# Performance work log

Hardware: AMD Instinct MI355X
Metric: run time of the kernel (lower is better)

## Reference

```python
import jax, jax.numpy as jnp
import numpy as np

B, T, V, H, F = 128, 20, 10000, 512, 49


def _uniform(key, shape, fan):
    s = 1.0 / np.sqrt(fan)
    return jax.random.uniform(key, shape, jnp.float32, -s, s)


def setup_inputs() -> dict:
    key = jax.random.key(0)
    ks = jax.random.split(key, 16)
    return {
        "caption_inputs": jax.random.randint(ks[0], (B, T), 0, V),
        "global_features": jax.random.normal(ks[1], (B, H), jnp.float32),
        "area_features": jax.random.normal(ks[2], (B, H, F), jnp.float32),
        "h0": jnp.zeros((B, H), jnp.float32),
        "c0": jnp.zeros((B, H), jnp.float32),
        # learned params
        "embedding": jax.random.normal(ks[3], (V, H), jnp.float32),
        "W_ih": _uniform(ks[4], (2 * H, 4 * H), H),   # LSTMCell input weights (x @ W_ih)
        "W_hh": _uniform(ks[5], (H, 4 * H), H),
        "b_ih": _uniform(ks[6], (4 * H,), H),
        "b_hh": _uniform(ks[7], (4 * H,), H),
        "Wv": _uniform(ks[8], (H, H), H),             # attention comp_visual
        "Wh": _uniform(ks[9], (H, H), H),             # attention comp_hidden
        "wo": _uniform(ks[10], (H,), H),              # attention output_layer
        "W_out": _uniform(ks[11], (2 * H, V), 2 * H), # decoder output layer
        "b_out": _uniform(ks[12], (V,), 2 * H),
    }


def reference(caption_inputs, global_features, area_features, h0, c0,
              embedding, W_ih, W_hh, b_ih, b_hh, Wv, Wh, wo, W_out, b_out):
    # Precompute attention visual projection (time-invariant): [B,F,H]
    feat = jnp.swapaxes(area_features, 1, 2)          # [B,F,H]
    Vproj = jnp.einsum('bfh,hk->bfk', feat, Wv)       # [B,F,H]
    bias = b_ih + b_hh

    def step(carry, tok):
        h, c = carry
        emb = embedding[tok]                           # [B,H]
        x = jnp.concatenate([emb, global_features], axis=1)   # [B,2H]
        gates = x @ W_ih + h @ W_hh + bias             # [B,4H]
        i, f, g, o = jnp.split(gates, 4, axis=1)
        c = jax.nn.sigmoid(f) * c + jax.nn.sigmoid(i) * jnp.tanh(g)
        h = jax.nn.sigmoid(o) * jnp.tanh(c)
        # spatial attention over F locations
        z = jnp.tanh(Vproj + (h @ Wh)[:, None, :])     # [B,F,H]
        scores = jnp.einsum('bfh,h->bf', z, wo)        # [B,F]
        alpha = jax.nn.softmax(scores, axis=1)
        attended = jnp.einsum('bhf,bf->bh', area_features, alpha)  # [B,H]
        out = jnp.concatenate([h, attended], axis=1) @ W_out + b_out  # [B,V]
        return (h, c), out

    (_, _), outs = jax.lax.scan(step, (h0, c0), caption_inputs.T)  # [T,B,V]
    return jnp.swapaxes(outs, 0, 1)                    # [B,T,V]
```

## Files before the change

kernel.cpp:

```cpp
#include <hip/hip_runtime.h>

#define B_ 128
#define T_ 20
#define V_ 10000
#define H_ 512
#define F_ 49
#define NBLK_ 128

typedef unsigned short u16;
typedef __attribute__((ext_vector_type(8))) short short8;
typedef __attribute__((ext_vector_type(4))) float floatx4;

#define GLOBAL_AS __attribute__((address_space(1)))
#define LDS_AS    __attribute__((address_space(3)))

__device__ inline void load_lds16(const void* g, void* l) {
    __builtin_amdgcn_global_load_lds((const GLOBAL_AS void*)g, (LDS_AS void*)l, 16, 0, 0);
}

__device__ inline u16 f2b(float v) {
    unsigned u = __builtin_bit_cast(unsigned, v);
    unsigned rounding = 0x7FFFu + ((u >> 16) & 1u);
    return (u16)((u + rounding) >> 16);
}
__device__ inline float b2f(u16 h) {
    unsigned u = ((unsigned)h) << 16;
    return __builtin_bit_cast(float, u);
}
__device__ inline float fast_tanh(float x) {
    return 1.f - 2.f / (__expf(2.f * x) + 1.f);
}
__device__ inline float sigm(float x) { return 1.f / (1.f + __expf(-x)); }

__device__ __forceinline__ void tr32(const float* __restrict__ src, u16* __restrict__ dst,
                                     int K, int N, int bx, int by, int tx, int ty,
                                     float (*tile)[33]) {
    int n0 = bx * 32, k0 = by * 32;
    #pragma unroll
    for (int i = 0; i < 32; i += 8) {
        int k = k0 + ty + i, n = n0 + tx;
        tile[ty + i][tx] = (k < K && n < N) ? src[(size_t)k * N + n] : 0.f;
    }
    __syncthreads();
    #pragma unroll
    for (int i = 0; i < 32; i += 8) {
        int n = n0 + ty + i, k = k0 + tx;
        if (n < N && k < K) dst[(size_t)n * K + k] = f2b(tile[tx][ty + i]);
    }
}

__global__ __launch_bounds__(256) void preamble(
        const float* __restrict__ W_ih, const float* __restrict__ W_hh,
        const float* __restrict__ Wv, const float* __restrict__ Wh,
        const float* __restrict__ W_out, const int* __restrict__ cap,
        const float* __restrict__ emb, const float* __restrict__ gf,
        const float* __restrict__ area, const float* __restrict__ h0,
        u16* __restrict__ WihT, u16* __restrict__ WhhT, u16* __restrict__ WvT,
        u16* __restrict__ WhT, u16* __restrict__ WoutT, u16* __restrict__ X,
        u16* __restrict__ feat, u16* __restrict__ Hall, int* __restrict__ bar) {
    __shared__ float tile[32][33];
    const int bid = blockIdx.x, tid = threadIdx.x;
    const int tx = tid & 31, ty = tid >> 5;

    if (bid < 2048) {
        int r = bid;                 tr32(W_ih, WihT, 1024, 2048, r % 64, r / 64, tx, ty, tile);
    } else if (bid < 3072) {
        int r = bid - 2048;          tr32(W_hh, WhhT, 512, 2048, r % 64, r / 64, tx, ty, tile);
    } else if (bid < 3328) {
        int r = bid - 3072;          tr32(Wv, WvT, 512, 512, r % 16, r / 16, tx, ty, tile);
    } else if (bid < 3584) {
        int r = bid - 3328;          tr32(Wh, WhT, 512, 512, r % 16, r / 16, tx, ty, tile);
    } else if (bid < 13600) {
        int r = bid - 3584;          tr32(W_out, WoutT, 1024, 10000, r % 313, r / 313, tx, ty, tile);
    } else if (bid < 16160) {
        int r = bid - 13600;
        int t = r / B_, b = r % B_;
        int tok = cap[b * T_ + t];
        for (int col = tid; col < 2 * H_; col += 256) {
            float v = (col < H_) ? emb[(size_t)tok * H_ + col] : gf[(size_t)b * H_ + (col - H_)];
            X[(size_t)r * (2 * H_) + col] = f2b(v);
        }
    } else if (bid < 19296) {
        int r = bid - 16160;
        #pragma unroll
        for (int k = 0; k < 4; ++k) {
            int idx = r * 1024 + k * 256 + tid;
            int h = idx & (H_ - 1);
            int bf_ = idx >> 9;
            int f = bf_ % F_, b = bf_ / F_;
            feat[idx] = f2b(area[((size_t)b * H_ + h) * F_ + f]);
        }
    } else {
        int r = bid - 19296;
        int i = r * 256 + tid;
        Hall[i] = f2b(h0[i]);
        if (r == 0) bar[tid] = 0;
    }
}

__device__ inline void grid_sync_mg(int* base, int ep) {
    __syncthreads();
    if (threadIdx.x == 0) {
        int old = __hip_atomic_fetch_add(&base[0], 1, __ATOMIC_ACQ_REL, __HIP_MEMORY_SCOPE_AGENT);
        if (old == ep * 32 - 1)
            __hip_atomic_store(&base[32], ep, __ATOMIC_RELEASE, __HIP_MEMORY_SCOPE_AGENT);
        while (__hip_atomic_load(&base[32], __ATOMIC_RELAXED, __HIP_MEMORY_SCOPE_AGENT) < ep)
            __builtin_amdgcn_s_sleep(2);
        (void)__hip_atomic_load(&base[32], __ATOMIC_ACQUIRE, __HIP_MEMORY_SCOPE_AGENT);
    }
    __syncthreads();
}

__global__ __launch_bounds__(256, 1) void decode_loop(
        const u16* __restrict__ WhhT, const float* __restrict__ Xin,
        const float* __restrict__ c0, u16* __restrict__ Hall,
        int* __restrict__ bar) {

    __shared__ __align__(16) u16 Whs[64 * 512];
    __shared__ __align__(16) u16 hstage[32 * 512];
    __shared__ float gl[4 * 32 * 16];
    __shared__ float csh[32 * 16];

    const int tid = threadIdx.x;
    const int wave = tid >> 6, lane = tid & 63;
    const int lm = lane & 15, q = lane >> 4;
    const int bid = blockIdx.x;
    const int jg = bid >> 2, mg = bid & 3;
    int* mybar = bar + mg * 64;

    const int lb0 = tid >> 4, jj = tid & 15;
    const int lb1 = lb0 + 16;
    const int grow0 = mg * 32 + lb0, grow1 = mg * 32 + lb1;
    const int j = jg * 16 + jj;

    #pragma unroll
    for (int i = 0; i < 16; ++i) {
        int row = i * 4 + wave;
        int g = row >> 4, lr = row & 15;
        int grr = g * H_ + jg * 16 + lr;
        load_lds16(WhhT + (size_t)grr * H_ + (size_t)(lane ^ (row & 7)) * 8,
                   (char*)Whs + row * 1024);
    }
    csh[tid] = c0[(size_t)grow0 * H_ + j];
    csh[tid + 256] = c0[(size_t)grow1 * H_ + j];

    float xf[8];
    {
        const float* x0 = Xin + (size_t)grow0 * (4 * H_);
        const float* x1 = Xin + (size_t)grow1 * (4 * H_);
        xf[0] = x0[j]; xf[1] = x0[H_ + j]; xf[2] = x0[2 * H_ + j]; xf[3] = x0[3 * H_ + j];
        xf[4] = x1[j]; xf[5] = x1[H_ + j]; xf[6] = x1[2 * H_ + j]; xf[7] = x1[3 * H_ + j];
    }

    for (int t = 0; t < T_; ++t) {
        const u16* hprev = Hall + (size_t)t * B_ * H_;
        u16* hnext = Hall + (size_t)(t + 1) * B_ * H_;

        #pragma unroll
        for (int it = 0; it < 8; ++it) {
            int row = it * 4 + wave;
            load_lds16(hprev + (size_t)(mg * 32 + row) * H_ + (size_t)(lane ^ (row & 7)) * 8,
                       (char*)hstage + row * 1024);
        }
        __syncthreads();

        floatx4 acc0 = {0.f, 0.f, 0.f, 0.f}, acc1 = {0.f, 0.f, 0.f, 0.f};
        #pragma unroll
        for (int kt = 0; kt < 16; ++kt) {
            int ch = kt * 4 + q;
            short8 a0 = *(const short8*)&hstage[(lm << 9) + ((ch ^ (lm & 7)) << 3)];
            short8 a1 = *(const short8*)&hstage[((16 + lm) << 9) + ((ch ^ (lm & 7)) << 3)];
            short8 bb = *(const short8*)&Whs[((wave * 16 + lm) << 9) + ((ch ^ (lm & 7)) << 3)];
            acc0 = __builtin_amdgcn_mfma_f32_16x16x32_bf16(a0, bb, acc0, 0, 0, 0);
            acc1 = __builtin_amdgcn_mfma_f32_16x16x32_bf16(a1, bb, acc1, 0, 0, 0);
        }
        #pragma unroll
        for (int r = 0; r < 4; ++r) {
            gl[wave * 512 + (q * 4 + r) * 16 + lm] = acc0[r];
            gl[wave * 512 + (16 + q * 4 + r) * 16 + lm] = acc1[r];
        }
        __syncthreads();

        float xc[8];
        #pragma unroll
        for (int i = 0; i < 8; ++i) xc[i] = xf[i];
        if (t + 1 < T_) {
            const float* x0 = Xin + ((size_t)(t + 1) * B_ + grow0) * (4 * H_);
            const float* x1 = Xin + ((size_t)(t + 1) * B_ + grow1) * (4 * H_);
            xf[0] = x0[j]; xf[1] = x0[H_ + j]; xf[2] = x0[2 * H_ + j]; xf[3] = x0[3 * H_ + j];
            xf[4] = x1[j]; xf[5] = x1[H_ + j]; xf[6] = x1[2 * H_ + j]; xf[7] = x1[3 * H_ + j];
        }

        {
            float gi = gl[0 * 512 + lb0 * 16 + jj] + xc[0];
            float gf = gl[1 * 512 + lb0 * 16 + jj] + xc[1];
            float gg = gl[2 * 512 + lb0 * 16 + jj] + xc[2];
            float go = gl[3 * 512 + lb0 * 16 + jj] + xc[3];
            float cn = sigm(gf) * csh[tid] + sigm(gi) * fast_tanh(gg);
            csh[tid] = cn;
            hnext[(size_t)grow0 * H_ + j] = f2b(sigm(go) * fast_tanh(cn));
        }
        {
            float gi = gl[0 * 512 + lb1 * 16 + jj] + xc[4];
            float gf = gl[1 * 512 + lb1 * 16 + jj] + xc[5];
            float gg = gl[2 * 512 + lb1 * 16 + jj] + xc[6];
            float go = gl[3 * 512 + lb1 * 16 + jj] + xc[7];
            float cn = sigm(gf) * csh[tid + 256] + sigm(gi) * fast_tanh(gg);
            csh[tid + 256] = cn;
            hnext[(size_t)grow1 * H_ + j] = f2b(sigm(go) * fast_tanh(cn));
        }

        if (t + 1 < T_) grid_sync_mg(mybar, t + 1);
    }
}

__global__ __launch_bounds__(256) void attn_post(
        const float* __restrict__ ahbuf, const u16* __restrict__ Vprojb,
        const u16* __restrict__ feat, const float* __restrict__ wo,
        const u16* __restrict__ Hall, u16* __restrict__ Hcat) {
    __shared__ __align__(16) u16 Vsh[F_ * H_];
    __shared__ __align__(16) u16 fsh[F_ * H_];
    __shared__ float ash[H_];
    __shared__ float wosh[H_];
    __shared__ float sc[64];

    const int tid = threadIdx.x;
    const int wave = tid >> 6, lane = tid & 63;
    const int b = blockIdx.x >> 1, th = blockIdx.x & 1;

    const short8* vsrc = (const short8*)(Vprojb + (size_t)b * F_ * H_);
    const short8* fsrc = (const short8*)(feat + (size_t)b * F_ * H_);
    for (int i = tid; i < F_ * H_ / 8; i += 256) {
        ((short8*)Vsh)[i] = vsrc[i];
        ((short8*)fsh)[i] = fsrc[i];
    }
    for (int i = tid; i < H_; i += 256) wosh[i] = wo[i];
    __syncthreads();

    for (int t = th * (T_ / 2); t < (th + 1) * (T_ / 2); ++t) {
        for (int i = tid; i < H_; i += 256)
            ash[i] = ahbuf[((size_t)t * B_ + b) * H_ + i];
        __syncthreads();

        for (int f = wave; f < F_; f += 4) {
            short8 vv = *(const short8*)&Vsh[f * H_ + lane * 8];
            float s = 0.f;
            #pragma unroll
            for (int e = 0; e < 8; ++e) {
                int h = lane * 8 + e;
                s += wosh[h] * fast_tanh(b2f((u16)vv[e]) + ash[h]);
            }
            #pragma unroll
            for (int off = 32; off; off >>= 1) s += __shfl_xor(s, off);
            if (lane == 0) sc[f] = s;
        }
        __syncthreads();

        if (tid < 64) {
            float v = (tid < F_) ? sc[tid] : -1e30f;
            float m = v;
            #pragma unroll
            for (int off = 32; off; off >>= 1) m = fmaxf(m, __shfl_xor(m, off));
            float e = (tid < F_) ? __expf(v - m) : 0.f;
            float sum = e;
            #pragma unroll
            for (int off = 32; off; off >>= 1) sum += __shfl_xor(sum, off);
            if (tid < F_) sc[tid] = e / sum;
        }
        __syncthreads();

        const size_t rowo = ((size_t)b * T_ + t) * (2 * H_);
        const short8* hrow = (const short8*)(Hall + ((size_t)(t + 1) * B_ + b) * H_);
        for (int i = tid; i < H_ / 8; i += 256)
            ((short8*)(Hcat + rowo))[i] = hrow[i];
        for (int h = tid; h < H_; h += 256) {
            float acc = 0.f;
            #pragma unroll
            for (int f = 0; f < F_; ++f) acc += b2f(fsh[f * H_ + h]) * sc[f];
            Hcat[rowo + H_ + h] = f2b(acc);
        }
        __syncthreads();
    }
}

template <int WRITE_BF16>
__device__ __forceinline__ void gemm2_body(
        const u16* __restrict__ A, int lda, const u16* __restrict__ Bt, int ldb,
        void* __restrict__ Cout, int ldc, const float* __restrict__ bias1,
        const float* __restrict__ bias2, int M, int N, int K, int bx, int by,
        u16* As, u16* Bs) {
    const int tid = threadIdx.x, wave = tid >> 6, lane = tid & 63;
    const int wr = wave >> 1, wc = wave & 1;
    const int lm = lane & 15, q = lane >> 4;
    const int m0 = bx * 128, n0 = by * 128;

    const int off = wave * 1024 + lane * 16;
    const int r0 = off >> 6;
    const int c0 = (off & 63) >> 1;

    const u16* gA0 = A + (size_t)(m0 + r0) * lda + c0;
    const u16* gA1 = A + (size_t)(m0 + r0 + 64) * lda + c0;
    int nb0 = n0 + r0;      if (nb0 > N - 1) nb0 = N - 1;
    int nb1 = n0 + r0 + 64; if (nb1 > N - 1) nb1 = N - 1;
    const u16* gB0 = Bt + (size_t)nb0 * ldb + c0;
    const u16* gB1 = Bt + (size_t)nb1 * ldb + c0;
    char* lA0 = (char*)As + wave * 1024;
    char* lA1 = (char*)As + 4096 + wave * 1024;
    char* lB0 = (char*)Bs + wave * 1024;
    char* lB1 = (char*)Bs + 4096 + wave * 1024;

    floatx4 acc[4][4];
    #pragma unroll
    for (int i = 0; i < 4; ++i)
        #pragma unroll
        for (int jq = 0; jq < 4; ++jq) acc[i][jq] = floatx4{0.f, 0.f, 0.f, 0.f};

    const int nkt = K >> 5;
    for (int kt = 0; kt < nkt; ++kt) {
        const int ko = kt * 32;
        load_lds16(gA0 + ko, lA0);
        load_lds16(gA1 + ko, lA1);
        load_lds16(gB0 + ko, lB0);
        load_lds16(gB1 + ko, lB1);
        __syncthreads();
        short8 af[4], bf[4];
        #pragma unroll
        for (int i = 0; i < 4; ++i)
            af[i] = *(const short8*)&As[(wr * 64 + i * 16 + lm) * 32 + q * 8];
        #pragma unroll
        for (int jq = 0; jq < 4; ++jq)
            bf[jq] = *(const short8*)&Bs[(wc * 64 + jq * 16 + lm) * 32 + q * 8];
        #pragma unroll
        for (int i = 0; i < 4; ++i)
            #pragma unroll
            for (int jq = 0; jq < 4; ++jq)
                acc[i][jq] = __builtin_amdgcn_mfma_f32_16x16x32_bf16(af[i], bf[jq], acc[i][jq], 0, 0, 0);
        __syncthreads();
    }

    #pragma unroll
    for (int i = 0; i < 4; ++i) {
        const int row = m0 + wr * 64 + i * 16 + q * 4;
        #pragma unroll
        for (int jq = 0; jq < 4; ++jq) {
            const int col = n0 + wc * 64 + jq * 16 + lm;
            if (col < N) {
                #pragma unroll
                for (int r = 0; r < 4; ++r) {
                    float v = acc[i][jq][r];
                    if (bias1) v += bias1[col];
                    if (bias2) v += bias2[col];
                    if (WRITE_BF16) ((u16*)Cout)[(size_t)(row + r) * ldc + col] = f2b(v);
                    else            ((float*)Cout)[(size_t)(row + r) * ldc + col] = v;
                }
            }
        }
    }
}

template <int WRITE_BF16>
__global__ __launch_bounds__(256) void gemm2(const u16* __restrict__ A, int lda,
                                             const u16* __restrict__ Bt, int ldb,
                                             void* __restrict__ Cout, int ldc,
                                             const float* __restrict__ bias1,
                                             const float* __restrict__ bias2,
                                             int M, int N, int K) {
    __shared__ __align__(16) u16 As[128 * 32];
    __shared__ __align__(16) u16 Bs[128 * 32];
    gemm2_body<WRITE_BF16>(A, lda, Bt, ldb, Cout, ldc, bias1, bias2, M, N, K,
                           blockIdx.x, blockIdx.y, As, Bs);
}

__global__ __launch_bounds__(256) void gemm_pair(
        const u16* __restrict__ X, const u16* __restrict__ WihT,
        float* __restrict__ Xin, const float* __restrict__ b_ih,
        const float* __restrict__ b_hh, const u16* __restrict__ feat,
        const u16* __restrict__ WvT, u16* __restrict__ Vprojb) {
    __shared__ __align__(16) u16 As[128 * 32];
    __shared__ __align__(16) u16 Bs[128 * 32];
    int bid = blockIdx.x;
    if (bid < 320) {
        gemm2_body<0>(X, 2 * H_, WihT, 2 * H_, Xin, 4 * H_, b_ih, b_hh,
                      T_ * B_, 4 * H_, 2 * H_, bid % 20, bid / 20, As, Bs);
    } else {
        int r = bid - 320;
        gemm2_body<1>(feat, H_, WvT, H_, Vprojb, H_, nullptr, nullptr,
                      B_ * F_, H_, H_, r % 49, r / 49, As, Bs);
    }
}

extern "C" void kernel_launch(void* const* d_in, const int* in_sizes, int n_in,
                              void* d_out, int out_size, void* d_ws, size_t ws_size,
                              hipStream_t stream) {
    const int*   cap   = (const int*)d_in[0];
    const float* gf    = (const float*)d_in[1];
    const float* area  = (const float*)d_in[2];
    const float* h0    = (const float*)d_in[3];
    const float* c0    = (const float*)d_in[4];
    const float* emb   = (const float*)d_in[5];
    const float* W_ih  = (const float*)d_in[6];
    const float* W_hh  = (const float*)d_in[7];
    const float* b_ih  = (const float*)d_in[8];
    const float* b_hh  = (const float*)d_in[9];
    const float* Wv    = (const float*)d_in[10];
    const float* Wh    = (const float*)d_in[11];
    const float* wo    = (const float*)d_in[12];
    const float* W_out = (const float*)d_in[13];
    const float* b_out = (const float*)d_in[14];
    float* out = (float*)d_out;

    char* p = (char*)d_ws;
    auto alloc = [&](size_t bytes) {
        char* q = p;
        p += (bytes + 255) & ~(size_t)255;
        return q;
    };
    u16*   X      = (u16*)alloc((size_t)T_ * B_ * 2 * H_ * 2);
    u16*   WihT   = (u16*)alloc((size_t)4 * H_ * 2 * H_ * 2);
    u16*   WhhT   = (u16*)alloc((size_t)4 * H_ * H_ * 2);
    u16*   WvT    = (u16*)alloc((size_t)H_ * H_ * 2);
    u16*   WhT    = (u16*)alloc((size_t)H_ * H_ * 2);
    u16*   WoutT  = (u16*)alloc((size_t)V_ * 2 * H_ * 2);
    u16*   feat   = (u16*)alloc((size_t)B_ * F_ * H_ * 2);
    float* Xin    = (float*)alloc((size_t)T_ * B_ * 4 * H_ * 4);
    u16*   Vprojb = (u16*)alloc((size_t)B_ * F_ * H_ * 2);
    float* ahbuf  = (float*)alloc((size_t)T_ * B_ * H_ * 4);
    u16*   Hall   = (u16*)alloc((size_t)(T_ + 1) * B_ * H_ * 2);
    int*   bar    = (int*)alloc(1024);
    u16*   Hcat   = (u16*)alloc((size_t)B_ * T_ * 2 * H_ * 2);

    preamble<<<19552, 256, 0, stream>>>(W_ih, W_hh, Wv, Wh, W_out, cap, emb, gf,
                                        area, h0, WihT, WhhT, WvT, WhT, WoutT,
                                        X, feat, Hall, bar);

    gemm_pair<<<516, 256, 0, stream>>>(X, WihT, Xin, b_ih, b_hh, feat, WvT, Vprojb);

    decode_loop<<<NBLK_, 256, 0, stream>>>(WhhT, Xin, c0, Hall, bar);

    gemm2<0><<<dim3(T_ * B_ / 128, H_ / 128), 256, 0, stream>>>(
        Hall + (size_t)B_ * H_, H_, WhT, H_, ahbuf, H_, nullptr, nullptr, T_ * B_, H_, H_);

    attn_post<<<2 * B_, 256, 0, stream>>>(ahbuf, Vprojb, feat, wo, Hall, Hcat);

    gemm2<0><<<dim3(T_ * B_ / 128, (V_ + 127) / 128), 256, 0, stream>>>(
        Hcat, 2 * H_, WoutT, 2 * H_, out, V_, b_out, nullptr, T_ * B_, V_, 2 * H_);
}
```

Baseline: 601.3 us.

## Double-buffer GEMM LDS tiles, remap blocks per XCD, tile the feature transpose

The GEMM body now prefetches the next K-slice into a second LDS buffer while MFMAs consume the current one, which removes one barrier per iteration. gemm2 remaps workgroup ids so that consecutive tiles land on the same XCD, aiming for better L2 reuse. The area-feature bf16 conversion now uses the 32x32 shared-memory transpose instead of strided scalar reads. The cost is doubled LDS use per block, which may reduce occupancy.

Measured after the change: 587.3 us. 2.3% less time.

```diff
diff --git a/kernel.cpp b/kernel.cpp
--- a/kernel.cpp
+++ b/kernel.cpp
@@ -34,18 +34,18 @@
 
 __device__ __forceinline__ void tr32(const float* __restrict__ src, u16* __restrict__ dst,
                                      int K, int N, int bx, int by, int tx, int ty,
-                                     float (*tile)[33]) {
+                                     float (*tl)[33]) {
     int n0 = bx * 32, k0 = by * 32;
     #pragma unroll
     for (int i = 0; i < 32; i += 8) {
         int k = k0 + ty + i, n = n0 + tx;
-        tile[ty + i][tx] = (k < K && n < N) ? src[(size_t)k * N + n] : 0.f;
+        tl[ty + i][tx] = (k < K && n < N) ? src[(size_t)k * N + n] : 0.f;
     }
     __syncthreads();
     #pragma unroll
     for (int i = 0; i < 32; i += 8) {
         int n = n0 + ty + i, k = k0 + tx;
-        if (n < N && k < K) dst[(size_t)n * K + k] = f2b(tile[tx][ty + i]);
+        if (n < N && k < K) dst[(size_t)n * K + k] = f2b(tl[tx][ty + i]);
     }
 }
 
@@ -58,20 +58,20 @@
         u16* __restrict__ WihT, u16* __restrict__ WhhT, u16* __restrict__ WvT,
         u16* __restrict__ WhT, u16* __restrict__ WoutT, u16* __restrict__ X,
         u16* __restrict__ feat, u16* __restrict__ Hall, int* __restrict__ bar) {
-    __shared__ float tile[32][33];
+    __shared__ float tl[32][33];
     const int bid = blockIdx.x, tid = threadIdx.x;
     const int tx = tid & 31, ty = tid >> 5;
 
     if (bid < 2048) {
-        int r = bid;                 tr32(W_ih, WihT, 1024, 2048, r % 64, r / 64, tx, ty, tile);
+        int r = bid;                 tr32(W_ih, WihT, 1024, 2048, r % 64, r / 64, tx, ty, tl);
     } else if (bid < 3072) {
-        int r = bid - 2048;          tr32(W_hh, WhhT, 512, 2048, r % 64, r / 64, tx, ty, tile);
+        int r = bid - 2048;          tr32(W_hh, WhhT, 512, 2048, r % 64, r / 64, tx, ty, tl);
     } else if (bid < 3328) {
-        int r = bid - 3072;          tr32(Wv, WvT, 512, 512, r % 16, r / 16, tx, ty, tile);
+        int r = bid - 3072;          tr32(Wv, WvT, 512, 512, r % 16, r / 16, tx, ty, tl);
     } else if (bid < 3584) {
-        int r = bid - 3328;          tr32(Wh, WhT, 512, 512, r % 16, r / 16, tx, ty, tile);
+        int r = bid - 3328;          tr32(Wh, WhT, 512, 512, r % 16, r / 16, tx, ty, tl);
     } else if (bid < 13600) {
-        int r = bid - 3584;          tr32(W_out, WoutT, 1024, 10000, r % 313, r / 313, tx, ty, tile);
+        int r = bid - 3584;          tr32(W_out, WoutT, 1024, 10000, r % 313, r / 313, tx, ty, tl);
     } else if (bid < 16160) {
         int r = bid - 13600;
         int t = r / B_, b = r % B_;
@@ -80,18 +80,14 @@
             float v = (col < H_) ? emb[(size_t)tok * H_ + col] : gf[(size_t)b * H_ + (col - H_)];
             X[(size_t)r * (2 * H_) + col] = f2b(v);
         }
-    } else if (bid < 19296) {
+    } else if (bid < 20256) {
         int r = bid - 16160;
-        #pragma unroll
-        for (int k = 0; k < 4; ++k) {
-            int idx = r * 1024 + k * 256 + tid;
-            int h = idx & (H_ - 1);
-            int bf_ = idx >> 9;
-            int f = bf_ % F_, b = bf_ / F_;
-            feat[idx] = f2b(area[((size_t)b * H_ + h) * F_ + f]);
-        }
+        int b = r >> 5, t32 = r & 31;
+        int fx = t32 & 1, hy = t32 >> 1;
+        tr32(area + (size_t)b * H_ * F_, feat + (size_t)b * F_ * H_,
+             H_, F_, fx, hy, tx, ty, tl);
     } else {
-        int r = bid - 19296;
+        int r = bid - 20256;
         int i = r * 256 + tid;
         Hall[i] = f2b(h0[i]);
         if (r == 0) bar[tid] = 0;
@@ -304,10 +300,6 @@
     int nb1 = n0 + r0 + 64; if (nb1 > N - 1) nb1 = N - 1;
     const u16* gB0 = Bt + (size_t)nb0 * ldb + c0;
     const u16* gB1 = Bt + (size_t)nb1 * ldb + c0;
-    char* lA0 = (char*)As + wave * 1024;
-    char* lA1 = (char*)As + 4096 + wave * 1024;
-    char* lB0 = (char*)Bs + wave * 1024;
-    char* lB1 = (char*)Bs + 4096 + wave * 1024;
 
     floatx4 acc[4][4];
     #pragma unroll
@@ -316,26 +308,41 @@
         for (int jq = 0; jq < 4; ++jq) acc[i][jq] = floatx4{0.f, 0.f, 0.f, 0.f};
 
     const int nkt = K >> 5;
+    {
+        load_lds16(gA0, (char*)As + wave * 1024);
+        load_lds16(gA1, (char*)As + 4096 + wave * 1024);
+        load_lds16(gB0, (char*)Bs + wave * 1024);
+        load_lds16(gB1, (char*)Bs + 4096 + wave * 1024);
+    }
+    __syncthreads();
+
+    int cur = 0;
     for (int kt = 0; kt < nkt; ++kt) {
-        const int ko = kt * 32;
-        load_lds16(gA0 + ko, lA0);
-        load_lds16(gA1 + ko, lA1);
-        load_lds16(gB0 + ko, lB0);
-        load_lds16(gB1 + ko, lB1);
-        __syncthreads();
+        if (kt + 1 < nkt) {
+            const int ko = (kt + 1) * 32;
+            char* dA = (char*)(As + (cur ^ 1) * 4096);
+            char* dB = (char*)(Bs + (cur ^ 1) * 4096);
+            load_lds16(gA0 + ko, dA + wave * 1024);
+            load_lds16(gA1 + ko, dA + 4096 + wave * 1024);
+            load_lds16(gB0 + ko, dB + wave * 1024);
+            load_lds16(gB1 + ko, dB + 4096 + wave * 1024);
+        }
+        const u16* Ab = As + cur * 4096;
+        const u16* Bb = Bs + cur * 4096;
         short8 af[4], bf[4];
         #pragma unroll
         for (int i = 0; i < 4; ++i)
-            af[i] = *(const short8*)&As[(wr * 64 + i * 16 + lm) * 32 + q * 8];
+            af[i] = *(const short8*)&Ab[(wr * 64 + i * 16 + lm) * 32 + q * 8];
         #pragma unroll
         for (int jq = 0; jq < 4; ++jq)
-            bf[jq] = *(const short8*)&Bs[(wc * 64 + jq * 16 + lm) * 32 + q * 8];
+            bf[jq] = *(const short8*)&Bb[(wc * 64 + jq * 16 + lm) * 32 + q * 8];
         #pragma unroll
         for (int i = 0; i < 4; ++i)
             #pragma unroll
             for (int jq = 0; jq < 4; ++jq)
                 acc[i][jq] = __builtin_amdgcn_mfma_f32_16x16x32_bf16(af[i], bf[jq], acc[i][jq], 0, 0, 0);
         __syncthreads();
+        cur ^= 1;
     }
 
     #pragma unroll
@@ -365,10 +372,16 @@
                                              const float* __restrict__ bias1,
                                              const float* __restrict__ bias2,
                                              int M, int N, int K) {
-    __shared__ __align__(16) u16 As[128 * 32];
-    __shared__ __align__(16) u16 Bs[128 * 32];
+    __shared__ __align__(16) u16 As[2 * 128 * 32];
+    __shared__ __align__(16) u16 Bs[2 * 128 * 32];
+    const int nbx = gridDim.x;
+    const int nwg = nbx * gridDim.y;
+    const int lin = blockIdx.x + blockIdx.y * nbx;
+    const int qq = nwg >> 3, rr = nwg & 7;
+    const int xcd = lin & 7, idx = lin >> 3;
+    const int wg = (xcd < rr ? xcd * (qq + 1) : rr * (qq + 1) + (xcd - rr) * qq) + idx;
     gemm2_body<WRITE_BF16>(A, lda, Bt, ldb, Cout, ldc, bias1, bias2, M, N, K,
-                           blockIdx.x, blockIdx.y, As, Bs);
+                           wg % nbx, wg / nbx, As, Bs);
 }
 
 __global__ __launch_bounds__(256) void gemm_pair(
@@ -376,8 +389,8 @@
         float* __restrict__ Xin, const float* __restrict__ b_ih,
         const float* __restrict__ b_hh, const u16* __restrict__ feat,
         const u16* __restrict__ WvT, u16* __restrict__ Vprojb) {
-    __shared__ __align__(16) u16 As[128 * 32];
-    __shared__ __align__(16) u16 Bs[128 * 32];
+    __shared__ __align__(16) u16 As[2 * 128 * 32];
+    __shared__ __align__(16) u16 Bs[2 * 128 * 32];
     int bid = blockIdx.x;
     if (bid < 320) {
         gemm2_body<0>(X, 2 * H_, WihT, 2 * H_, Xin, 4 * H_, b_ih, b_hh,
@@ -429,7 +442,7 @@
     int*   bar    = (int*)alloc(1024);
     u16*   Hcat   = (u16*)alloc((size_t)B_ * T_ * 2 * H_ * 2);
 
-    preamble<<<19552, 256, 0, stream>>>(W_ih, W_hh, Wv, Wh, W_out, cap, emb, gf,
+    preamble<<<20512, 256, 0, stream>>>(W_ih, W_hh, Wv, Wh, W_out, cap, emb, gf,
                                         area, h0, WihT, WhhT, WvT, WhT, WoutT,
                                         X, feat, Hall, bar);
 
```
